# Kernel optimization log

Hardware: AMD Instinct MI355X
Metric: run time of the kernel (lower is better)

The kernel has to match this reference:

```python
import jax, jax.numpy as jnp
import numpy as np

NUM_VECTORS = 8192
DIM = 64

def setup_inputs() -> dict:
    key = jax.random.key(0)
    kx, kw = jax.random.split(key)
    x = jax.random.normal(kx, (8, 4096, DIM), dtype=jnp.float32)
    W = jax.random.normal(kw, (NUM_VECTORS, DIM), dtype=jnp.float32)
    return {"x": x, "W": W}

def reference(x, W):
    # x: [B, S, C] channels_last (ndim==3 -> channels_first=False)
    shape = x.shape
    flat = x.reshape(-1, shape[-1])  # [N, C]
    # cdist + argmin: argmin of squared euclidean distance is identical to argmin of cdist
    x2 = jnp.sum(flat * flat, axis=1, keepdims=True)          # [N, 1]
    w2 = jnp.sum(W * W, axis=1)                                # [K]
    d2 = x2 - 2.0 * (flat @ W.T) + w2                          # [N, K] dominant intermediate
    indices = jnp.argmin(d2, axis=1)                           # [N]
    z = W[indices]                                             # gather [N, C]
    # losses (use_ema=True -> codebook_loss = 0)
    commitment_loss = jnp.mean((z - jax.lax.stop_gradient(flat)) ** 2)
    codebook_loss = jnp.zeros_like(commitment_loss)
    # straight-through estimator
    z_st = flat + jax.lax.stop_gradient(z - flat)
    # perplexity: scatter one-hot counts -> mean -> entropy
    n = flat.shape[0]
    counts = jnp.zeros((NUM_VECTORS,), dtype=jnp.float32).at[indices].add(1.0)
    avg_probs = counts / n
    perplexity = jnp.exp(-jnp.sum(avg_probs * jnp.log(avg_probs + 1e-10)))
    z_out = z_st.reshape(shape)
    return (z_out, codebook_loss, commitment_loss, perplexity)
```

## Files before the change

kernel.cpp:

```cpp
#include <hip/hip_runtime.h>
#include <math.h>

#define N_ROWS 32768
#define K_CODES 8192
#define DIM 64
#define CHUNKS 4
#define CPC (K_CODES / CHUNKS)
#define TILES (CPC / 32)

using half8  = __attribute__((ext_vector_type(8))) _Float16;
using f32x16 = __attribute__((ext_vector_type(16))) float;

#define WS_W2     0
#define WS_COUNTS 32768
#define WS_CSUM   65536
#define WS_BEST   65552
#define WS_X2     327696
#define WS_WHL    458768

__device__ __forceinline__ void gload_lds16(const _Float16* g, _Float16* l) {
    __builtin_amdgcn_global_load_lds(
        (const __attribute__((address_space(1))) void*)g,
        (__attribute__((address_space(3))) void*)l, 16, 0, 0);
}

__global__ __launch_bounds__(256) void vq_prep(const float* __restrict__ W,
                                               const float* __restrict__ x,
                                               _Float16* __restrict__ whl,
                                               float* __restrict__ w2g,
                                               float* __restrict__ x2g,
                                               unsigned long long* __restrict__ best,
                                               int* __restrict__ counts,
                                               float* __restrict__ csum) {
    int g = blockIdx.x * 256 + threadIdx.x;
    int code = g >> 6, k = g & 63;
    float w = W[g];
    _Float16 h  = (_Float16)w;
    _Float16 lo = (_Float16)(w - (float)h);
    whl[(size_t)code * 128 + k]      = h;
    whl[(size_t)code * 128 + 64 + k] = lo;
    float s = w * w;
    #pragma unroll
    for (int off = 32; off; off >>= 1) s += __shfl_down(s, off);
    if (k == 0) w2g[code] = s;
    float4 xv = *(const float4*)(x + (size_t)g * 4);
    float ss = xv.x * xv.x + xv.y * xv.y + xv.z * xv.z + xv.w * xv.w;
    #pragma unroll
    for (int off = 8; off; off >>= 1) ss += __shfl_down(ss, off);
    if ((g & 15) == 0) x2g[g >> 4] = ss;
    if (g < N_ROWS)  best[g] = ~0ULL;
    if (g < K_CODES) counts[g] = 0;
    if (g == 0)      *csum = 0.f;
}

__global__ __launch_bounds__(256, 4) void vq_mfma(const float* __restrict__ x,
                                                  const _Float16* __restrict__ whl,
                                                  const float* __restrict__ w2g,
                                                  unsigned long long* __restrict__ best) {
    __shared__ __align__(16) _Float16 lds[2][4096];
    __shared__ float w2l[CPC];

    const int t     = threadIdx.x;
    const int wv    = t >> 6;
    const int l     = t & 63;
    const int ln31  = l & 31;
    const int lhalf = l >> 5;
    const int chunk = blockIdx.x & (CHUNKS - 1);
    const int rblk  = blockIdx.x / CHUNKS;
    const int rowb  = rblk * 128 + wv * 32;
    const int cbase = chunk * CPC;

    for (int i = t; i < CPC; i += 256) w2l[i] = w2g[cbase + i];

    half8 ahi[4], alo[4];
    {
        const float* xr = x + (size_t)(rowb + ln31) * DIM + lhalf * 8;
        #pragma unroll
        for (int kt = 0; kt < 4; ++kt) {
            float4 a0 = *(const float4*)(xr + kt * 16);
            float4 a1 = *(const float4*)(xr + kt * 16 + 4);
            float fa[8] = {a0.x, a0.y, a0.z, a0.w, a1.x, a1.y, a1.z, a1.w};
            #pragma unroll
            for (int j = 0; j < 8; ++j) {
                _Float16 h = (_Float16)fa[j];
                ahi[kt][j] = h;
                alo[kt][j] = (_Float16)(fa[j] - (float)h);
            }
        }
    }

    const _Float16* srcp[2];
    int ldsG[2];
    #pragma unroll
    for (int p = 0; p < 2; ++p) {
        int q = p * 4 + wv;
        srcp[p] = whl + (size_t)(cbase + ln31) * 128 + ((q & 1) * 8 + lhalf + 2 * (q >> 1)) * 8;
        ldsG[p] = (p * 256 + wv * 64) * 8;
    }

    float bv[16];
    int   bi[16];
    #pragma unroll
    for (int s2 = 0; s2 < 16; ++s2) { bv[s2] = 3.4e38f; bi[s2] = 0; }

    #pragma unroll
    for (int p = 0; p < 2; ++p) gload_lds16(srcp[p], &lds[0][0] + ldsG[p]);
    __syncthreads();

    int cur = 0;
    for (int tile = 0; tile < TILES; ++tile) {
        if (tile < TILES - 1) {
            #pragma unroll
            for (int p = 0; p < 2; ++p)
                gload_lds16(srcp[p] + (tile + 1) * 4096, &lds[0][0] + (cur ^ 1) * 4096 + ldsG[p]);
        }
        const float w2v = w2l[tile * 32 + ln31];
        const _Float16* lb = &lds[0][0] + cur * 4096;

        f32x16 accA = {}, accB = {};
        __builtin_amdgcn_s_setprio(1);
        #pragma unroll
        for (int kt = 0; kt < 4; ++kt) {
            half8 bh = *(const half8*)(lb + ((kt * 2 + 0) * 64 + l) * 8);
            half8 bl = *(const half8*)(lb + ((kt * 2 + 1) * 64 + l) * 8);
            accA = __builtin_amdgcn_mfma_f32_32x32x16_f16(ahi[kt], bh, accA, 0, 0, 0);
            accB = __builtin_amdgcn_mfma_f32_32x32x16_f16(alo[kt], bh, accB, 0, 0, 0);
            accB = __builtin_amdgcn_mfma_f32_32x32x16_f16(ahi[kt], bl, accB, 0, 0, 0);
        }
        __builtin_amdgcn_s_setprio(0);

        const int cc = cbase + tile * 32 + ln31;
        #pragma unroll
        for (int s2 = 0; s2 < 16; ++s2) {
            float sA = fmaf(-2.f, accA[s2], fmaf(-2.f, accB[s2], w2v));
            if (sA < bv[s2]) { bv[s2] = sA; bi[s2] = cc; }
        }
        __syncthreads();
        cur ^= 1;
    }

    #pragma unroll
    for (int s2 = 0; s2 < 16; ++s2) {
        unsigned uk = __float_as_uint(bv[s2]);
        uk = (uk >> 31) ? ~uk : (uk | 0x80000000u);
        unsigned long long key = ((unsigned long long)uk << 32) | (unsigned)bi[s2];
        #pragma unroll
        for (int off = 16; off; off >>= 1) {
            unsigned long long o = __shfl_xor(key, off);
            key = (o < key) ? o : key;
        }
        if (ln31 == 0) {
            int rl = (s2 & 3) + 8 * (s2 >> 2) + 4 * lhalf;
            atomicMin(&best[rowb + rl], key);
        }
    }
}

__global__ __launch_bounds__(256) void vq_gather(const float* __restrict__ W,
                                                 const unsigned long long* __restrict__ best,
                                                 const float* __restrict__ x2g,
                                                 float* __restrict__ zout,
                                                 int* __restrict__ counts,
                                                 float* __restrict__ csum) {
    int t   = threadIdx.x;
    int row = blockIdx.x * 64 + (t >> 2);
    int seg = t & 3;
    unsigned long long key = best[row];
    int idx = (int)(key & 0xFFFFFFFFULL);

    const float* wrow = W    + (size_t)idx * DIM + seg * 16;
    float*       zrow = zout + (size_t)row * DIM + seg * 16;
    #pragma unroll
    for (int j = 0; j < 16; j += 4) *(float4*)(zrow + j) = *(const float4*)(wrow + j);

    float local = 0.f;
    if (seg == 0) {
        atomicAdd(&counts[idx], 1);
        unsigned uk = (unsigned)(key >> 32);
        unsigned ob = (uk & 0x80000000u) ? (uk & 0x7FFFFFFFu) : ~uk;
        local = x2g[row] + __uint_as_float(ob);
    }
    #pragma unroll
    for (int off = 32; off; off >>= 1) local += __shfl_down(local, off);
    if ((t & 63) == 0) atomicAdd(csum, local);
}

__global__ __launch_bounds__(256) void vq_final(const int* __restrict__ counts,
                                                const float* __restrict__ csum,
                                                float* __restrict__ out3) {
    __shared__ float sh[4];
    float e = 0.f;
    for (int i = threadIdx.x; i < K_CODES; i += 256) {
        float p = (float)counts[i] * (1.0f / N_ROWS);
        e += p * logf(p + 1e-10f);
    }
    #pragma unroll
    for (int off = 32; off; off >>= 1) e += __shfl_down(e, off);
    if ((threadIdx.x & 63) == 0) sh[threadIdx.x >> 6] = e;
    __syncthreads();
    if (threadIdx.x == 0) {
        float tot = sh[0] + sh[1] + sh[2] + sh[3];
        out3[0] = 0.f;
        out3[1] = csum[0] * (1.0f / ((float)N_ROWS * DIM));
        out3[2] = expf(-tot);
    }
}

extern "C" void kernel_launch(void* const* d_in, const int* in_sizes, int n_in,
                              void* d_out, int out_size, void* d_ws, size_t ws_size,
                              hipStream_t stream) {
    (void)in_sizes; (void)n_in; (void)out_size; (void)ws_size;
    const float* x = (const float*)d_in[0];
    const float* W = (const float*)d_in[1];
    float* zout = (float*)d_out;
    float* out3 = (float*)d_out + (size_t)N_ROWS * DIM;

    float*              w2g    = (float*)((char*)d_ws + WS_W2);
    int*                counts = (int*)((char*)d_ws + WS_COUNTS);
    float*              csum   = (float*)((char*)d_ws + WS_CSUM);
    unsigned long long* best   = (unsigned long long*)((char*)d_ws + WS_BEST);
    float*              x2g    = (float*)((char*)d_ws + WS_X2);
    _Float16*           whl    = (_Float16*)((char*)d_ws + WS_WHL);

    vq_prep  <<<K_CODES * DIM / 256,     256, 0, stream>>>(W, x, whl, w2g, x2g, best, counts, csum);
    vq_mfma  <<<(N_ROWS / 128) * CHUNKS, 256, 0, stream>>>(x, whl, w2g, best);
    vq_gather<<<N_ROWS / 64,             256, 0, stream>>>(W, best, x2g, zout, counts, csum);
    vq_final <<<1,                       256, 0, stream>>>(counts, csum, out3);
}
```

Measured before the change: 160.7 us.

## Merge split-precision accumulators, double code chunks, raise occupancy, parallelize final reduction

The three hi/lo MFMA products now go into one accumulator, so each tile holds 16 fewer accumulator registers and needs one fewer FMA per element. The launch bound moves from 4 to 6 waves per SIMD, and the codebook is split into 8 chunks instead of 4, doubling the number of blocks. The final entropy reduction now runs across 32 blocks that combine through atomics and a last-block-done counter, replacing a single-block loop. The shared accumulator chain serializes the MFMAs within each k-step, and more chunks mean more atomic min updates to the best array.

```diff
diff --git a/kernel.cpp b/kernel.cpp
--- a/kernel.cpp
+++ b/kernel.cpp
@@ -4,7 +4,7 @@
 #define N_ROWS 32768
 #define K_CODES 8192
 #define DIM 64
-#define CHUNKS 4
+#define CHUNKS 8
 #define CPC (K_CODES / CHUNKS)
 #define TILES (CPC / 32)
 
@@ -14,6 +14,8 @@
 #define WS_W2     0
 #define WS_COUNTS 32768
 #define WS_CSUM   65536
+#define WS_ESUM   65540
+#define WS_DONE   65544
 #define WS_BEST   65552
 #define WS_X2     327696
 #define WS_WHL    458768
@@ -31,7 +33,8 @@
                                                float* __restrict__ x2g,
                                                unsigned long long* __restrict__ best,
                                                int* __restrict__ counts,
-                                               float* __restrict__ csum) {
+                                               float* __restrict__ scal,
+                                               int* __restrict__ done) {
     int g = blockIdx.x * 256 + threadIdx.x;
     int code = g >> 6, k = g & 63;
     float w = W[g];
@@ -50,10 +53,10 @@
     if ((g & 15) == 0) x2g[g >> 4] = ss;
     if (g < N_ROWS)  best[g] = ~0ULL;
     if (g < K_CODES) counts[g] = 0;
-    if (g == 0)      *csum = 0.f;
-}
-
-__global__ __launch_bounds__(256, 4) void vq_mfma(const float* __restrict__ x,
+    if (g == 0) { scal[0] = 0.f; scal[1] = 0.f; *done = 0; }
+}
+
+__global__ __launch_bounds__(256, 6) void vq_mfma(const float* __restrict__ x,
                                                   const _Float16* __restrict__ whl,
                                                   const float* __restrict__ w2g,
                                                   unsigned long long* __restrict__ best) {
@@ -112,27 +115,28 @@
         if (tile < TILES - 1) {
             #pragma unroll
             for (int p = 0; p < 2; ++p)
-                gload_lds16(srcp[p] + (tile + 1) * 4096, &lds[0][0] + (cur ^ 1) * 4096 + ldsG[p]);
+                gload_lds16(srcp[p] + (size_t)(tile + 1) * 4096,
+                            &lds[0][0] + (cur ^ 1) * 4096 + ldsG[p]);
         }
         const float w2v = w2l[tile * 32 + ln31];
         const _Float16* lb = &lds[0][0] + cur * 4096;
 
-        f32x16 accA = {}, accB = {};
+        f32x16 acc = {};
         __builtin_amdgcn_s_setprio(1);
         #pragma unroll
         for (int kt = 0; kt < 4; ++kt) {
             half8 bh = *(const half8*)(lb + ((kt * 2 + 0) * 64 + l) * 8);
             half8 bl = *(const half8*)(lb + ((kt * 2 + 1) * 64 + l) * 8);
-            accA = __builtin_amdgcn_mfma_f32_32x32x16_f16(ahi[kt], bh, accA, 0, 0, 0);
-            accB = __builtin_amdgcn_mfma_f32_32x32x16_f16(alo[kt], bh, accB, 0, 0, 0);
-            accB = __builtin_amdgcn_mfma_f32_32x32x16_f16(ahi[kt], bl, accB, 0, 0, 0);
+            acc = __builtin_amdgcn_mfma_f32_32x32x16_f16(ahi[kt], bh, acc, 0, 0, 0);
+            acc = __builtin_amdgcn_mfma_f32_32x32x16_f16(alo[kt], bh, acc, 0, 0, 0);
+            acc = __builtin_amdgcn_mfma_f32_32x32x16_f16(ahi[kt], bl, acc, 0, 0, 0);
         }
         __builtin_amdgcn_s_setprio(0);
 
         const int cc = cbase + tile * 32 + ln31;
         #pragma unroll
         for (int s2 = 0; s2 < 16; ++s2) {
-            float sA = fmaf(-2.f, accA[s2], fmaf(-2.f, accB[s2], w2v));
+            float sA = fmaf(-2.f, acc[s2], w2v);
             if (sA < bv[s2]) { bv[s2] = sA; bi[s2] = cc; }
         }
         __syncthreads();
@@ -186,23 +190,28 @@
 }
 
 __global__ __launch_bounds__(256) void vq_final(const int* __restrict__ counts,
-                                                const float* __restrict__ csum,
+                                                float* __restrict__ scal,
+                                                int* __restrict__ done,
                                                 float* __restrict__ out3) {
     __shared__ float sh[4];
-    float e = 0.f;
-    for (int i = threadIdx.x; i < K_CODES; i += 256) {
-        float p = (float)counts[i] * (1.0f / N_ROWS);
-        e += p * logf(p + 1e-10f);
-    }
+    int g = blockIdx.x * 256 + threadIdx.x;
+    float p = (float)counts[g] * (1.0f / N_ROWS);
+    float e = p * logf(p + 1e-10f);
     #pragma unroll
     for (int off = 32; off; off >>= 1) e += __shfl_down(e, off);
     if ((threadIdx.x & 63) == 0) sh[threadIdx.x >> 6] = e;
     __syncthreads();
     if (threadIdx.x == 0) {
-        float tot = sh[0] + sh[1] + sh[2] + sh[3];
-        out3[0] = 0.f;
-        out3[1] = csum[0] * (1.0f / ((float)N_ROWS * DIM));
-        out3[2] = expf(-tot);
+        atomicAdd(&scal[1], sh[0] + sh[1] + sh[2] + sh[3]);
+        __threadfence();
+        int old = atomicAdd(done, 1);
+        if (old == 31) {
+            float es = atomicAdd(&scal[1], 0.f);
+            float cs = atomicAdd(&scal[0], 0.f);
+            out3[0] = 0.f;
+            out3[1] = cs * (1.0f / ((float)N_ROWS * DIM));
+            out3[2] = expf(-es);
+        }
     }
 }
 
@@ -217,13 +226,14 @@
 
     float*              w2g    = (float*)((char*)d_ws + WS_W2);
     int*                counts = (int*)((char*)d_ws + WS_COUNTS);
-    float*              csum   = (float*)((char*)d_ws + WS_CSUM);
+    float*              scal   = (float*)((char*)d_ws + WS_CSUM);
+    int*                done   = (int*)((char*)d_ws + WS_DONE);
     unsigned long long* best   = (unsigned long long*)((char*)d_ws + WS_BEST);
     float*              x2g    = (float*)((char*)d_ws + WS_X2);
     _Float16*           whl    = (_Float16*)((char*)d_ws + WS_WHL);
 
-    vq_prep  <<<K_CODES * DIM / 256,     256, 0, stream>>>(W, x, whl, w2g, x2g, best, counts, csum);
+    vq_prep  <<<K_CODES * DIM / 256,     256, 0, stream>>>(W, x, whl, w2g, x2g, best, counts, scal, done);
     vq_mfma  <<<(N_ROWS / 128) * CHUNKS, 256, 0, stream>>>(x, whl, w2g, best);
-    vq_gather<<<N_ROWS / 64,             256, 0, stream>>>(W, best, x2g, zout, counts, csum);
-    vq_final <<<1,                       256, 0, stream>>>(counts, csum, out3);
-}
+    vq_gather<<<N_ROWS / 64,             256, 0, stream>>>(W, best, x2g, zout, counts, &scal[0]);
+    vq_final <<<K_CODES / 256,           256, 0, stream>>>(counts, scal, done, out3);
+}
```

Measured after the change: 267.1 us. +66.2%, slower.
